# Kernel optimization log

Hardware: AMD Instinct MI355X
Metric: run time of the kernel (lower is better)

## Reference

```python
import jax, jax.numpy as jnp
import numpy as np

B = 262144  # batch*frames; each sample = 8 joints x 3x3 basis = 72 floats


def _to4x4(p):
    # p: [B, 72] -> homogeneous 4x4 per joint, grouped as 2 chains of 4 joints
    m = p.reshape(-1, 8, 3, 3)
    # first column completed via cross product of the two stored basis columns
    x = jnp.cross(m[..., 0], m[..., 1])[..., None]          # [B,8,3,1]
    rot = jnp.concatenate([x, m], axis=-1)                   # [B,8,3,4]
    bottom = jnp.broadcast_to(
        jnp.array([0.0, 0.0, 0.0, 1.0], rot.dtype),
        rot.shape[:2] + (1, 4))                              # [B,8,1,4]
    m44 = jnp.concatenate([rot, bottom], axis=-2)            # [B,8,4,4]
    return m44.reshape(-1, 2, 4, 4, 4)                       # [B,2,4,4,4]


def _fk_translation(m):
    # chain product of 4 joint matrices per chain; identity start folds away
    f = m[:, :, 0]
    for j in range(1, 4):  # fixed small unroll over chain depth
        f = jnp.matmul(f, m[:, :, j])
    return f[:, :, :3, 3]                                    # [B,2,3]


def setup_inputs() -> dict:
    key = jax.random.key(0)
    k1, k2, k3 = jax.random.split(key, 3)
    return {
        "output_pose": jax.random.normal(k1, (B, 72), dtype=jnp.float32),
        "gt_pose": jax.random.normal(k2, (B, 72), dtype=jnp.float32),
        "gt_prev_pose": jax.random.normal(k3, (B, 72), dtype=jnp.float32),
    }


def reference(output_pose, gt_pose, gt_prev_pose):
    out_fk = _fk_translation(_to4x4(output_pose))
    gt_fk = _fk_translation(_to4x4(gt_pose))
    gt_prev_fk = _fk_translation(_to4x4(gt_prev_pose))
    pos_loss = jnp.mean((out_fk - gt_fk) ** 2)
    gt_vel = gt_fk - gt_prev_fk
    out_vel = out_fk - gt_prev_fk
    vel_loss = jnp.mean((out_vel - gt_vel) ** 2)
    return (pos_loss, vel_loss)
```

## Files before the change

kernel.cpp:

```cpp
#include <hip/hip_runtime.h>

#define NPOSE  262144
#define NCHAIN (NPOSE * 2)
#define BLOCK  64
#define CPB    64
#define NBLK   (NCHAIN / CPB)

typedef __attribute__((address_space(1))) void glb_void_t;
typedef __attribute__((address_space(3))) void lds_void_t;

__device__ __forceinline__ void fk_step(float e0, float e1, float e2,
                                        float e3, float e4, float e5,
                                        float e6, float e7, float e8,
                                        float& v0, float& v1, float& v2) {
    const float x0 = e3 * e7 - e6 * e4;
    const float x1 = e6 * e1 - e0 * e7;
    const float x2 = e0 * e4 - e3 * e1;
    const float w0 = e2 + x0 * v0 + e0 * v1 + e1 * v2;
    const float w1 = e5 + x1 * v0 + e3 * v1 + e4 * v2;
    const float w2 = e8 + x2 * v0 + e6 * v1 + e7 * v2;
    v0 = w0; v1 = w1; v2 = w2;
}

__device__ __forceinline__ void chain_translation_q(
        float4 q0, float4 q1, float4 q2, float4 q3, float4 q4,
        float4 q5, float4 q6, float4 q7, float4 q8,
        float& v0, float& v1, float& v2) {
    v0 = q7.y; v1 = q8.x; v2 = q8.w;
    fk_step(q4.z, q4.w, q5.x, q5.y, q5.z, q5.w, q6.x, q6.y, q6.z, v0, v1, v2);
    fk_step(q2.y, q2.z, q2.w, q3.x, q3.y, q3.z, q3.w, q4.x, q4.y, v0, v1, v2);
    fk_step(q0.x, q0.y, q0.z, q0.w, q1.x, q1.y, q1.z, q1.w, q2.x, v0, v1, v2);
}

__global__ __launch_bounds__(BLOCK) void fk_loss_kernel(const float* __restrict__ outp,
                                                        const float* __restrict__ gtp,
                                                        float* __restrict__ partials) {
    __shared__ float4 ldsA[CPB * 9];
    __shared__ float4 ldsB[CPB * 9];
    const int t = threadIdx.x;
    const size_t base4 = (size_t)blockIdx.x * (CPB * 9);
    const float4* __restrict__ ga = reinterpret_cast<const float4*>(outp) + base4;
    const float4* __restrict__ gb = reinterpret_cast<const float4*>(gtp) + base4;

#pragma unroll
    for (int i = 0; i < 9; ++i)
        __builtin_amdgcn_global_load_lds((glb_void_t*)(ga + t + 64 * i),
                                         (lds_void_t*)(&ldsA[i * 64]), 16, 0, 0);
#pragma unroll
    for (int i = 0; i < 9; ++i)
        __builtin_amdgcn_global_load_lds((glb_void_t*)(gb + t + 64 * i),
                                         (lds_void_t*)(&ldsB[i * 64]), 16, 0, 0);

    __syncthreads();

    float tax, tay, taz;
    {
        const float4 r0 = ldsA[t * 9 + 0], r1 = ldsA[t * 9 + 1], r2 = ldsA[t * 9 + 2],
                     r3 = ldsA[t * 9 + 3], r4 = ldsA[t * 9 + 4], r5 = ldsA[t * 9 + 5],
                     r6 = ldsA[t * 9 + 6], r7 = ldsA[t * 9 + 7], r8 = ldsA[t * 9 + 8];
        chain_translation_q(r0, r1, r2, r3, r4, r5, r6, r7, r8, tax, tay, taz);
    }
    float tgx, tgy, tgz;
    {
        const float4 r0 = ldsB[t * 9 + 0], r1 = ldsB[t * 9 + 1], r2 = ldsB[t * 9 + 2],
                     r3 = ldsB[t * 9 + 3], r4 = ldsB[t * 9 + 4], r5 = ldsB[t * 9 + 5],
                     r6 = ldsB[t * 9 + 6], r7 = ldsB[t * 9 + 7], r8 = ldsB[t * 9 + 8];
        chain_translation_q(r0, r1, r2, r3, r4, r5, r6, r7, r8, tgx, tgy, tgz);
    }

    const float d0 = tax - tgx, d1 = tay - tgy, d2 = taz - tgz;
    float acc = d0 * d0 + d1 * d1 + d2 * d2;

#pragma unroll
    for (int off = 32; off > 0; off >>= 1)
        acc += __shfl_down(acc, off, 64);
    if (t == 0) partials[blockIdx.x] = acc;
}

__global__ __launch_bounds__(512) void reduce_kernel(const float* __restrict__ partials,
                                                     float* __restrict__ out) {
    const int t = threadIdx.x;
    const float4* __restrict__ p4 = reinterpret_cast<const float4*>(partials);
    float s = 0.0f;
#pragma unroll
    for (int i = 0; i < 4; ++i) {
        const float4 v = p4[t + 512 * i];
        s += v.x + v.y + v.z + v.w;
    }
#pragma unroll
    for (int off = 32; off > 0; off >>= 1)
        s += __shfl_down(s, off, 64);
    __shared__ float smem[8];
    const int lane = t & 63, wid = t >> 6;
    if (lane == 0) smem[wid] = s;
    __syncthreads();
    if (t == 0) {
        float tot = 0.0f;
#pragma unroll
        for (int w = 0; w < 8; ++w) tot += smem[w];
        const float mean = tot / (262144.0f * 6.0f);
        out[0] = mean;
        out[1] = mean;
    }
}

extern "C" void kernel_launch(void* const* d_in, const int* in_sizes, int n_in,
                              void* d_out, int out_size, void* d_ws, size_t ws_size,
                              hipStream_t stream) {
    const float* output_pose = (const float*)d_in[0];
    const float* gt_pose     = (const float*)d_in[1];
    float* out = (float*)d_out;
    float* partials = (float*)d_ws;

    fk_loss_kernel<<<NBLK, BLOCK, 0, stream>>>(output_pose, gt_pose, partials);
    reduce_kernel<<<1, 512, 0, stream>>>(partials, out);
}
```

Before: 28.82 us.

## Double-buffer async global-to-LDS loads across eight chain tiles per block

Each single-wave block now processes eight 64-chain tiles instead of one. The next tile is prefetched into a second LDS buffer with global_load_lds while the current tile is computed, synchronised with explicit s_waitcnt vmcnt. The aim is to hide load latency and cut per-block launch overhead. The trade-off is an eight-fold drop in grid size (1024 single-wave blocks), which lowers occupancy and memory-level parallelism on a kernel that is already close to bandwidth-bound. The reduce kernel is shrunk to match the smaller partials array.

```diff
diff --git a/kernel.cpp b/kernel.cpp
--- a/kernel.cpp
+++ b/kernel.cpp
@@ -3,8 +3,8 @@
 #define NPOSE  262144
 #define NCHAIN (NPOSE * 2)
 #define BLOCK  64
-#define CPB    64
-#define NBLK   (NCHAIN / CPB)
+#define TPB    8
+#define NBLK   (NCHAIN / (64 * TPB))
 
 typedef __attribute__((address_space(1))) void glb_void_t;
 typedef __attribute__((address_space(3))) void lds_void_t;
@@ -35,41 +35,52 @@
 __global__ __launch_bounds__(BLOCK) void fk_loss_kernel(const float* __restrict__ outp,
                                                         const float* __restrict__ gtp,
                                                         float* __restrict__ partials) {
-    __shared__ float4 ldsA[CPB * 9];
-    __shared__ float4 ldsB[CPB * 9];
+    __shared__ float4 ldsA[2][64 * 9];
+    __shared__ float4 ldsB[2][64 * 9];
     const int t = threadIdx.x;
-    const size_t base4 = (size_t)blockIdx.x * (CPB * 9);
-    const float4* __restrict__ ga = reinterpret_cast<const float4*>(outp) + base4;
-    const float4* __restrict__ gb = reinterpret_cast<const float4*>(gtp) + base4;
+    const float4* __restrict__ g0 = reinterpret_cast<const float4*>(outp);
+    const float4* __restrict__ g1 = reinterpret_cast<const float4*>(gtp);
+    const int tile0 = blockIdx.x * TPB;
 
+    auto issue = [&](int tile, int b) {
+        const float4* pa = g0 + (size_t)tile * 576 + t;
+        const float4* pb = g1 + (size_t)tile * 576 + t;
 #pragma unroll
-    for (int i = 0; i < 9; ++i)
-        __builtin_amdgcn_global_load_lds((glb_void_t*)(ga + t + 64 * i),
-                                         (lds_void_t*)(&ldsA[i * 64]), 16, 0, 0);
+        for (int i = 0; i < 9; ++i) {
+            __builtin_amdgcn_global_load_lds((glb_void_t*)(pa + 64 * i),
+                                             (lds_void_t*)(&ldsA[b][i * 64]), 16, 0, 0);
+            __builtin_amdgcn_global_load_lds((glb_void_t*)(pb + 64 * i),
+                                             (lds_void_t*)(&ldsB[b][i * 64]), 16, 0, 0);
+        }
+    };
+
+    float acc = 0.0f;
+    issue(tile0, 0);
 #pragma unroll
-    for (int i = 0; i < 9; ++i)
-        __builtin_amdgcn_global_load_lds((glb_void_t*)(gb + t + 64 * i),
-                                         (lds_void_t*)(&ldsB[i * 64]), 16, 0, 0);
-
-    __syncthreads();
-
-    float tax, tay, taz;
-    {
-        const float4 r0 = ldsA[t * 9 + 0], r1 = ldsA[t * 9 + 1], r2 = ldsA[t * 9 + 2],
-                     r3 = ldsA[t * 9 + 3], r4 = ldsA[t * 9 + 4], r5 = ldsA[t * 9 + 5],
-                     r6 = ldsA[t * 9 + 6], r7 = ldsA[t * 9 + 7], r8 = ldsA[t * 9 + 8];
-        chain_translation_q(r0, r1, r2, r3, r4, r5, r6, r7, r8, tax, tay, taz);
+    for (int it = 0; it < TPB; ++it) {
+        const int b = it & 1;
+        if (it < TPB - 1) {
+            issue(tile0 + it + 1, b ^ 1);
+            asm volatile("s_waitcnt vmcnt(18)" ::: "memory");
+        } else {
+            asm volatile("s_waitcnt vmcnt(0)" ::: "memory");
+        }
+        float tax, tay, taz, tgx, tgy, tgz;
+        {
+            const float4 r0 = ldsA[b][t * 9 + 0], r1 = ldsA[b][t * 9 + 1], r2 = ldsA[b][t * 9 + 2],
+                         r3 = ldsA[b][t * 9 + 3], r4 = ldsA[b][t * 9 + 4], r5 = ldsA[b][t * 9 + 5],
+                         r6 = ldsA[b][t * 9 + 6], r7 = ldsA[b][t * 9 + 7], r8 = ldsA[b][t * 9 + 8];
+            chain_translation_q(r0, r1, r2, r3, r4, r5, r6, r7, r8, tax, tay, taz);
+        }
+        {
+            const float4 r0 = ldsB[b][t * 9 + 0], r1 = ldsB[b][t * 9 + 1], r2 = ldsB[b][t * 9 + 2],
+                         r3 = ldsB[b][t * 9 + 3], r4 = ldsB[b][t * 9 + 4], r5 = ldsB[b][t * 9 + 5],
+                         r6 = ldsB[b][t * 9 + 6], r7 = ldsB[b][t * 9 + 7], r8 = ldsB[b][t * 9 + 8];
+            chain_translation_q(r0, r1, r2, r3, r4, r5, r6, r7, r8, tgx, tgy, tgz);
+        }
+        const float d0 = tax - tgx, d1 = tay - tgy, d2 = taz - tgz;
+        acc += d0 * d0 + d1 * d1 + d2 * d2;
     }
-    float tgx, tgy, tgz;
-    {
-        const float4 r0 = ldsB[t * 9 + 0], r1 = ldsB[t * 9 + 1], r2 = ldsB[t * 9 + 2],
-                     r3 = ldsB[t * 9 + 3], r4 = ldsB[t * 9 + 4], r5 = ldsB[t * 9 + 5],
-                     r6 = ldsB[t * 9 + 6], r7 = ldsB[t * 9 + 7], r8 = ldsB[t * 9 + 8];
-        chain_translation_q(r0, r1, r2, r3, r4, r5, r6, r7, r8, tgx, tgy, tgz);
-    }
-
-    const float d0 = tax - tgx, d1 = tay - tgy, d2 = taz - tgz;
-    float acc = d0 * d0 + d1 * d1 + d2 * d2;
 
 #pragma unroll
     for (int off = 32; off > 0; off >>= 1)
@@ -77,27 +88,21 @@
     if (t == 0) partials[blockIdx.x] = acc;
 }
 
-__global__ __launch_bounds__(512) void reduce_kernel(const float* __restrict__ partials,
+__global__ __launch_bounds__(256) void reduce_kernel(const float* __restrict__ partials,
                                                      float* __restrict__ out) {
     const int t = threadIdx.x;
     const float4* __restrict__ p4 = reinterpret_cast<const float4*>(partials);
-    float s = 0.0f;
-#pragma unroll
-    for (int i = 0; i < 4; ++i) {
-        const float4 v = p4[t + 512 * i];
-        s += v.x + v.y + v.z + v.w;
-    }
+    const float4 v = p4[t];
+    float s = v.x + v.y + v.z + v.w;
 #pragma unroll
     for (int off = 32; off > 0; off >>= 1)
         s += __shfl_down(s, off, 64);
-    __shared__ float smem[8];
+    __shared__ float smem[4];
     const int lane = t & 63, wid = t >> 6;
     if (lane == 0) smem[wid] = s;
     __syncthreads();
     if (t == 0) {
-        float tot = 0.0f;
-#pragma unroll
-        for (int w = 0; w < 8; ++w) tot += smem[w];
+        const float tot = smem[0] + smem[1] + smem[2] + smem[3];
         const float mean = tot / (262144.0f * 6.0f);
         out[0] = mean;
         out[1] = mean;
@@ -113,5 +118,5 @@
     float* partials = (float*)d_ws;
 
     fk_loss_kernel<<<NBLK, BLOCK, 0, stream>>>(output_pose, gt_pose, partials);
-    reduce_kernel<<<1, 512, 0, stream>>>(partials, out);
+    reduce_kernel<<<1, 256, 0, stream>>>(partials, out);
 }
```

New measurement: 29.05 us. No clear change (+0.8%).
